# Kernel optimization log

Measured on AMD Instinct MI355X. Metric: run time of the kernel, lower is better.

## Reference

```python
import jax, jax.numpy as jnp
import numpy as np

GRID_LON = 17  # idx = lat*17 + lon in original code


def setup_inputs() -> dict:
    key = jax.random.key(0)
    ks = jax.random.split(key, 16)
    B, S, L = 512, 256, 64
    DIM_RHO, DIM_C, HID = 256, 128, 512
    N_LAT, N_LON = 17, GRID_LON

    rho = jax.random.normal(ks[0], (B, S, DIM_RHO), dtype=jnp.float32)
    c = jax.random.normal(ks[1], (1, DIM_C, N_LAT, N_LON), dtype=jnp.float32)
    w = jax.random.uniform(ks[2], (B, S), dtype=jnp.float32, minval=1e-3, maxval=1.0)
    l = jax.random.uniform(ks[3], (B,), dtype=jnp.float32, minval=0.1, maxval=10.0)
    roads = jax.random.randint(ks[4], (B, L), 0, N_LAT * N_LON)
    lon_idx = jax.random.randint(ks[5], (B, L), 0, N_LON)
    lat_idx = jax.random.randint(ks[6], (B, L), 0, N_LAT)

    sc = lambda fan_in: 1.0 / np.sqrt(fan_in)
    # f2: MLP(128, 256, 128) with selu
    f2_W1 = jax.random.uniform(ks[7], (DIM_C, 256), jnp.float32, -sc(DIM_C), sc(DIM_C))
    f2_b1 = jnp.zeros((256,), jnp.float32)
    f2_W2 = jax.random.uniform(ks[8], (256, DIM_C), jnp.float32, -sc(256), sc(256))
    f2_b2 = jnp.zeros((DIM_C,), jnp.float32)
    # f: MLP2(dim_rho + dim_c, hidden, 1) with selu (use_selu=True)
    fin = DIM_RHO + DIM_C
    f_W1 = jax.random.uniform(ks[9], (fin, HID), jnp.float32, -sc(fin), sc(fin))
    f_b1 = jnp.zeros((HID,), jnp.float32)
    f_W21 = jax.random.uniform(ks[10], (HID, 1), jnp.float32, -sc(HID), sc(HID))
    f_b21 = jnp.zeros((1,), jnp.float32)
    f_W22 = jax.random.uniform(ks[11], (HID, 1), jnp.float32, -sc(HID), sc(HID))
    f_b22 = jnp.zeros((1,), jnp.float32)

    return dict(rho=rho, c=c, w=w, l=l, roads=roads, lon_idx=lon_idx,
                lat_idx=lat_idx, f2_W1=f2_W1, f2_b1=f2_b1, f2_W2=f2_W2,
                f2_b2=f2_b2, f_W1=f_W1, f_b1=f_b1, f_W21=f_W21, f_b21=f_b21,
                f_W22=f_W22, f_b22=f_b22)


def reference(rho, c, w, l, roads, lon_idx, lat_idx,
              f2_W1, f2_b1, f2_W2, f2_b2,
              f_W1, f_b1, f_W21, f_b21, f_W22, f_b22):
    # c: (1, dim_c, n_lat, n_lon) -> (n_lat*n_lon, dim_c)
    c3 = jnp.squeeze(c, 0)                       # (dim_c, n_lat, n_lon)
    c_flat = jnp.transpose(c3, (1, 2, 0)).reshape(-1, c3.shape[0])  # (cells, dim_c)

    # ragged gather-mean, vectorized: (B, L) cell indices -> (B, dim_c)
    idx = lat_idx * GRID_LON + lon_idx           # (B, L)
    c_traj = jnp.mean(c_flat[idx], axis=1)       # (B, dim_c)

    # f2: selu MLP (dropout inactive / eval mode)
    h = jax.nn.selu(c_traj @ f2_W1 + f2_b1)
    c_tr = h @ f2_W2 + f2_b2                     # (B, dim_c)

    # broadcast over seq and concat with rho
    S = rho.shape[1]
    c_exp = jnp.broadcast_to(c_tr[:, None, :], (rho.shape[0], S, c_tr.shape[-1]))
    x = jnp.concatenate([rho, c_exp], axis=2)    # (B, S, dim_rho + dim_c)

    # f (MLP2, selu since use_selu=True)
    h1 = jax.nn.selu(x @ f_W1 + f_b1)            # (B, S, hidden)
    logm = (h1 @ f_W21 + f_b21)[..., 0]          # (B, S)
    logv = (h1 @ f_W22 + f_b22)[..., 0]          # (B, S)

    logw = jnp.log(w)
    logm_agg = jax.nn.logsumexp(logm + logw, axis=1)       # (B,)
    logv_agg = jax.nn.logsumexp(logv + 2.0 * logw, axis=1) # (B,)
    logl = jnp.log(l)
    log_mu = logl - logm_agg
    log_lambda = logl - 3.0 * logm_agg - logv_agg
    return (log_mu, log_lambda)
```

## Files before the change

### kernel.cpp

```cpp
#include <hip/hip_runtime.h>
#include <hip/hip_bf16.h>

typedef short bf16x8 __attribute__((ext_vector_type(8)));
typedef short bf16x4 __attribute__((ext_vector_type(4)));
typedef float f32x4 __attribute__((ext_vector_type(4)));
typedef _Float16 half4 __attribute__((ext_vector_type(4)));

__device__ __forceinline__ short f2bf(float f) {
    union { float f; unsigned u; } v; v.f = f;
    unsigned r = (v.u + 0x7FFFu + ((v.u >> 16) & 1u)) >> 16;
    return (short)r;
}

__device__ __forceinline__ float selu_f(float x) {
    const float scale = 1.0507009873554805f;
    const float sa = 1.0507009873554805f * 1.6732632423543772f;
    return x > 0.f ? scale * x : sa * (__expf(x) - 1.f);
}

__device__ __forceinline__ void gld_lds16(const char* g, char* l) {
    __builtin_amdgcn_global_load_lds(
        (const __attribute__((address_space(1))) unsigned int*)g,
        (__attribute__((address_space(3))) unsigned int*)l, 16, 0, 0);
}

__global__ void __launch_bounds__(512) prep_all_kernel(
    const float* __restrict__ c, const int* __restrict__ lat_idx,
    const int* __restrict__ lon_idx,
    const float* __restrict__ f2W1, const float* __restrict__ f2b1,
    const float* __restrict__ f2W2, const float* __restrict__ f2b2,
    const float* __restrict__ fW1, const float* __restrict__ fb1,
    const float* __restrict__ fW21, const float* __restrict__ fW22,
    short* __restrict__ w1img, _Float16* __restrict__ wvec,
    float* __restrict__ cbias)
{
    const int bid = blockIdx.x;
    const int t = threadIdx.x;

    if (bid < 512) {
        __shared__ int cells[64];
        __shared__ float ctraj[128];
        __shared__ float hbuf[256];
        __shared__ float ctrf[128];
        const int b = bid;

        if (t < 64) cells[t] = lat_idx[b * 64 + t] * 17 + lon_idx[b * 64 + t];
        __syncthreads();

        if (t < 128) {
            float s = 0.f;
            #pragma unroll 8
            for (int j = 0; j < 64; ++j) s += c[t * 289 + cells[j]];
            ctraj[t] = s * (1.f / 64.f);
        }
        __syncthreads();

        if (t < 256) {
            float acc = f2b1[t];
            #pragma unroll 8
            for (int i = 0; i < 128; ++i) acc += ctraj[i] * f2W1[i * 256 + t];
            hbuf[t] = selu_f(acc);
        }
        __syncthreads();

        if (t < 128) {
            float acc = f2b2[t];
            #pragma unroll 8
            for (int i = 0; i < 256; ++i) acc += hbuf[i] * f2W2[i * 128 + t];
            ctrf[t] = acc;
        }
        __syncthreads();

        float acc = fb1[t];
        #pragma unroll 8
        for (int i = 0; i < 128; ++i) acc += ctrf[i] * fW1[(256 + i) * 512 + t];
        cbias[b * 512 + t] = acc;
    } else if (bid < 768) {
        int I = (bid - 512) * 512 + t;
        int e = I & 7;
        int lane = (I >> 3) & 63;
        int cg = (I >> 9) & 31;
        int kc = I >> 14;
        int col = cg * 16 + (lane & 15);
        int k = kc * 32 + ((lane >> 4) << 3) + e;
        w1img[I] = f2bf(fW1[k * 512 + col]);
    } else {
        int I = (bid - 768) * 512 + t;
        int e = I & 3;
        int lane = (I >> 2) & 63;
        int nc = I >> 8;
        int l15 = lane & 15, hi = lane >> 4;
        int n = nc * 16 + hi * 4 + e;
        float v = (l15 == 0) ? fW21[n] : (l15 == 1 ? fW22[n] : 0.f);
        wvec[I] = (_Float16)v;
    }
}

__global__ void __launch_bounds__(1024, 4) fused_gemm_kernel(
    const float* __restrict__ rho, const short* __restrict__ w1img,
    const float* __restrict__ cbias, const _Float16* __restrict__ wvec,
    float* __restrict__ plm, float* __restrict__ plv)
{
    __shared__ __align__(16) char smem[131072];

    const int tid  = threadIdx.x;
    const int lane = tid & 63;
    const int wid  = tid >> 6;
    const int wr   = wid >> 3;
    const int wc2  = wid & 7;
    const int l15  = lane & 15;
    const int hi   = lane >> 4;

    const int b  = blockIdx.x >> 1;
    const int s0 = (blockIdx.x & 1) << 7;

    const int rg_t = tid >> 7;
    const int ln_t = (tid >> 1) & 63;
    const int h_t  = tid & 1;
    const float* prA = rho + (size_t)(b * 256 + s0 + rg_t * 16 + (ln_t & 15)) * 256
                           + ((ln_t >> 4) << 3) + h_t * 4;
    const int awoff = ((rg_t * 64 + ln_t) << 4) + (h_t << 3);

    const char* wsrc = (const char*)w1img;

    f32x4 acc[4][4];
    #pragma unroll
    for (int nf = 0; nf < 4; ++nf)
        #pragma unroll
        for (int sf = 0; sf < 4; ++sf)
            acc[nf][sf] = (f32x4){0.f, 0.f, 0.f, 0.f};

    float4 pf0, pf1;

    {
        const char* bs0 = wsrc + (wid * 2) * 1024 + lane * 16;
        char* bd0 = smem + 24576 + (wid * 2) * 1024;
        gld_lds16(bs0, bd0);
        gld_lds16(bs0 + 1024, bd0 + 1024);
        pf0 = *(const float4*)(prA);
        const char* bs1 = wsrc + 32768 + (wid * 2) * 1024 + lane * 16;
        char* bd1 = smem + 24576 + 32768 + (wid * 2) * 1024;
        gld_lds16(bs1, bd1);
        gld_lds16(bs1 + 1024, bd1 + 1024);
        pf1 = *(const float4*)(prA + 8);
    }

#define CHUNK(I, PFX)                                                          \
    {                                                                          \
        {          \
          bf16x4 hh;                                                           \
          hh[0] = f2bf(PFX.x); hh[1] = f2bf(PFX.y);                            \
          hh[2] = f2bf(PFX.z); hh[3] = f2bf(PFX.w);                            \
          *(bf16x4*)(smem + ((I) % 3) * 8192 + awoff) = hh; }                  \
        if ((I) + 2 <= 7) {    \
            const char* bs = wsrc + ((I) + 2) * 32768 + (wid * 2) * 1024       \
                             + lane * 16;                                      \
            char* bd = smem + 24576 + (((I) + 2) % 3) * 32768                  \
                       + (wid * 2) * 1024;                                     \
            gld_lds16(bs, bd);                                                 \
            gld_lds16(bs + 1024, bd + 1024);                                   \
            PFX = *(const float4*)(prA + ((I) + 2) * 8);                       \
        }                                                                      \
        asm volatile("s_waitcnt lgkmcnt(0)" ::: "memory");                     \
        __builtin_amdgcn_s_barrier();                                          \
        __builtin_amdgcn_sched_barrier(0);                                     \
        {                                                                      \
            bf16x8 aF[4], bF[4];                                               \
            const char* ab = smem + ((I) % 3) * 8192;                          \
            const char* bb = smem + 24576 + ((I) % 3) * 32768;                 \
            _Pragma("unroll")                                                  \
            for (int sf = 0; sf < 4; ++sf)                                     \
                aF[sf] = *(const bf16x8*)(ab + (((wr * 4 + sf) * 64 + lane) << 4)); \
            _Pragma("unroll")                                                  \
            for (int nf = 0; nf < 4; ++nf)                                     \
                bF[nf] = *(const bf16x8*)(bb + (((wc2 * 4 + nf) * 64 + lane) << 4)); \
            _Pragma("unroll")                                                  \
            for (int nf = 0; nf < 4; ++nf)                                     \
                _Pragma("unroll")                                              \
                for (int sf = 0; sf < 4; ++sf)                                 \
                    acc[nf][sf] = __builtin_amdgcn_mfma_f32_16x16x32_bf16(     \
                        bF[nf], aF[sf], acc[nf][sf], 0, 0, 0);                 \
        }                                                                      \
        __builtin_amdgcn_sched_barrier(0);                                     \
        __builtin_amdgcn_s_barrier();                                          \
    }

    CHUNK(0, pf0)
    CHUNK(1, pf1)
    CHUNK(2, pf0)
    CHUNK(3, pf1)
    CHUNK(4, pf0)
    CHUNK(5, pf1)
    CHUNK(6, pf0)
    CHUNK(7, pf1)
#undef CHUNK

    f32x4 rd[4];
    #pragma unroll
    for (int sf = 0; sf < 4; ++sf) rd[sf] = (f32x4){0.f, 0.f, 0.f, 0.f};

    #pragma unroll
    for (int nf = 0; nf < 4; ++nf) {
        f32x4 cbf = *(const f32x4*)(cbias + b * 512 + wc2 * 64 + nf * 16 + hi * 4);
        half4 wv = *(const half4*)(wvec + (size_t)(wc2 * 4 + nf) * 256 + lane * 4);
        #pragma unroll
        for (int sf = 0; sf < 4; ++sf) {
            half4 pa;
            #pragma unroll
            for (int q = 0; q < 4; ++q)
                pa[q] = (_Float16)selu_f(acc[nf][sf][q] + cbf[q]);
            rd[sf] = __builtin_amdgcn_mfma_f32_16x16x16f16(pa, wv, rd[sf], 0, 0, 0);
        }
    }

    float* redM = (float*)(smem + 122880);
    float* redV = (float*)(smem + 126976);
    if (l15 == 0) {
        #pragma unroll
        for (int sf = 0; sf < 4; ++sf)
            *(f32x4*)&redM[wc2 * 128 + wr * 64 + sf * 16 + hi * 4] = rd[sf];
    } else if (l15 == 1) {
        #pragma unroll
        for (int sf = 0; sf < 4; ++sf)
            *(f32x4*)&redV[wc2 * 128 + wr * 64 + sf * 16 + hi * 4] = rd[sf];
    }

    __syncthreads();
    size_t obase = (size_t)b * 256 + s0;
    if (tid < 128) {
        float s = 0.f;
        #pragma unroll
        for (int j = 0; j < 8; ++j) s += redM[j * 128 + tid];
        plm[obase + tid] = s;
    } else if (tid < 256) {
        int rr = tid - 128;
        float s = 0.f;
        #pragma unroll
        for (int j = 0; j < 8; ++j) s += redV[j * 128 + rr];
        plv[obase + rr] = s;
    }
}

__global__ void __launch_bounds__(64) finalize_kernel(
    const float* __restrict__ plm, const float* __restrict__ plv,
    const float* __restrict__ w, const float* __restrict__ l,
    const float* __restrict__ b21p, const float* __restrict__ b22p,
    float* __restrict__ out)
{
    const int b = blockIdx.x;
    const int lane = threadIdx.x;
    const float b21 = b21p[0], b22 = b22p[0];

    float a1[4], a2[4];
    float m1 = -1e30f, m2 = -1e30f;
    #pragma unroll
    for (int i = 0; i < 4; ++i) {
        int s = i * 64 + lane;
        float lw = logf(w[b * 256 + s]);
        a1[i] = plm[b * 256 + s] + b21 + lw;
        a2[i] = plv[b * 256 + s] + b22 + 2.f * lw;
        m1 = fmaxf(m1, a1[i]);
        m2 = fmaxf(m2, a2[i]);
    }
    #pragma unroll
    for (int m = 1; m < 64; m <<= 1) {
        m1 = fmaxf(m1, __shfl_xor(m1, m));
        m2 = fmaxf(m2, __shfl_xor(m2, m));
    }
    float s1 = 0.f, s2 = 0.f;
    #pragma unroll
    for (int i = 0; i < 4; ++i) {
        s1 += expf(a1[i] - m1);
        s2 += expf(a2[i] - m2);
    }
    #pragma unroll
    for (int m = 1; m < 64; m <<= 1) {
        s1 += __shfl_xor(s1, m);
        s2 += __shfl_xor(s2, m);
    }
    if (lane == 0) {
        float lm_agg = m1 + logf(s1);
        float lv_agg = m2 + logf(s2);
        float logl = logf(l[b]);
        out[b]       = logl - lm_agg;
        out[512 + b] = logl - 3.f * lm_agg - lv_agg;
    }
}

extern "C" void kernel_launch(void* const* d_in, const int* in_sizes, int n_in,
                              void* d_out, int out_size, void* d_ws, size_t ws_size,
                              hipStream_t stream) {
    const float* rho     = (const float*)d_in[0];
    const float* c       = (const float*)d_in[1];
    const float* w       = (const float*)d_in[2];
    const float* l       = (const float*)d_in[3];
    const int*   lon_idx = (const int*)d_in[5];
    const int*   lat_idx = (const int*)d_in[6];
    const float* f2W1    = (const float*)d_in[7];
    const float* f2b1    = (const float*)d_in[8];
    const float* f2W2    = (const float*)d_in[9];
    const float* f2b2    = (const float*)d_in[10];
    const float* fW1     = (const float*)d_in[11];
    const float* fb1     = (const float*)d_in[12];
    const float* fW21    = (const float*)d_in[13];
    const float* fb21    = (const float*)d_in[14];
    const float* fW22    = (const float*)d_in[15];
    const float* fb22    = (const float*)d_in[16];
    float* out = (float*)d_out;

    char* ws = (char*)d_ws;
    float*     cbias = (float*)(ws);
    short*     w1img = (short*)(ws + 1048576);
    float*     plm   = (float*)(ws + 1310720);
    float*     plv   = (float*)(ws + 1835008);
    _Float16*  wvec  = (_Float16*)(ws + 2359296);

    prep_all_kernel<<<784, 512, 0, stream>>>(c, lat_idx, lon_idx,
                                             f2W1, f2b1, f2W2, f2b2,
                                             fW1, fb1, fW21, fW22,
                                             w1img, wvec, cbias);
    fused_gemm_kernel<<<1024, 1024, 0, stream>>>(rho, w1img, cbias, wvec,
                                                 plm, plv);
    finalize_kernel<<<512, 64, 0, stream>>>(plm, plv, w, l, fb21, fb22, out);
}
```

Baseline: 99.94 us.

## Split hidden dimension across blocks with smaller double-buffered tiles

```diff
diff --git a/kernel.cpp b/kernel.cpp
--- a/kernel.cpp
+++ b/kernel.cpp
@@ -2,7 +2,6 @@
 #include <hip/hip_bf16.h>
 
 typedef short bf16x8 __attribute__((ext_vector_type(8)));
-typedef short bf16x4 __attribute__((ext_vector_type(4)));
 typedef float f32x4 __attribute__((ext_vector_type(4)));
 typedef _Float16 half4 __attribute__((ext_vector_type(4)));
 
@@ -96,32 +95,32 @@
     }
 }
 
-__global__ void __launch_bounds__(1024, 4) fused_gemm_kernel(
+__global__ void __launch_bounds__(512, 4) fused_gemm_kernel(
     const float* __restrict__ rho, const short* __restrict__ w1img,
     const float* __restrict__ cbias, const _Float16* __restrict__ wvec,
-    float* __restrict__ plm, float* __restrict__ plv)
+    float* __restrict__ plmP, float* __restrict__ plvP)
 {
-    __shared__ __align__(16) char smem[131072];
+    __shared__ __align__(16) char smem[53248];
 
     const int tid  = threadIdx.x;
     const int lane = tid & 63;
     const int wid  = tid >> 6;
-    const int wr   = wid >> 3;
-    const int wc2  = wid & 7;
+    const int wr   = wid >> 2;
+    const int wc   = wid & 3;
     const int l15  = lane & 15;
     const int hi   = lane >> 4;
 
-    const int b  = blockIdx.x >> 1;
-    const int s0 = (blockIdx.x & 1) << 7;
-
-    const int rg_t = tid >> 7;
-    const int ln_t = (tid >> 1) & 63;
-    const int h_t  = tid & 1;
-    const float* prA = rho + (size_t)(b * 256 + s0 + rg_t * 16 + (ln_t & 15)) * 256
-                           + ((ln_t >> 4) << 3) + h_t * 4;
-    const int awoff = ((rg_t * 64 + ln_t) << 4) + (h_t << 3);
-
-    const char* wsrc = (const char*)w1img;
+    const int b  = blockIdx.x >> 2;
+    const int s0 = ((blockIdx.x >> 1) & 1) << 7;
+    const int nh = blockIdx.x & 1;
+
+    const float* prA = rho + (size_t)(b * 256 + s0 + (tid >> 6) * 16 + (tid & 15)) * 256
+                           + (((tid & 63) >> 4) << 3);
+    char* aw = smem + tid * 16;
+
+    const char* wsrc = (const char*)w1img
+                     + ((size_t)(nh * 16 + wid * 2) * 64 + lane) * 16;
+    char* bw = smem + 16384 + (wid * 2) * 1024;
 
     f32x4 acc[4][4];
     #pragma unroll
@@ -130,69 +129,63 @@
         for (int sf = 0; sf < 4; ++sf)
             acc[nf][sf] = (f32x4){0.f, 0.f, 0.f, 0.f};
 
-    float4 pf0, pf1;
-
-    {
-        const char* bs0 = wsrc + (wid * 2) * 1024 + lane * 16;
-        char* bd0 = smem + 24576 + (wid * 2) * 1024;
-        gld_lds16(bs0, bd0);
-        gld_lds16(bs0 + 1024, bd0 + 1024);
-        pf0 = *(const float4*)(prA);
-        const char* bs1 = wsrc + 32768 + (wid * 2) * 1024 + lane * 16;
-        char* bd1 = smem + 24576 + 32768 + (wid * 2) * 1024;
-        gld_lds16(bs1, bd1);
-        gld_lds16(bs1 + 1024, bd1 + 1024);
-        pf1 = *(const float4*)(prA + 8);
-    }
-
-#define CHUNK(I, PFX)                                                          \
+    float4 e0, e1, o0, o1;
+
+    e0 = *(const float4*)(prA);
+    e1 = *(const float4*)(prA + 4);
+    gld_lds16(wsrc, smem + 16384 + (wid * 2) * 1024);
+    gld_lds16(wsrc + 1024, smem + 16384 + (wid * 2) * 1024 + 1024);
+
+#define CHUNK(I, C0, C1, N0, N1, LAST)                                         \
     {                                                                          \
-        {          \
-          bf16x4 hh;                                                           \
-          hh[0] = f2bf(PFX.x); hh[1] = f2bf(PFX.y);                            \
-          hh[2] = f2bf(PFX.z); hh[3] = f2bf(PFX.w);                            \
-          *(bf16x4*)(smem + ((I) % 3) * 8192 + awoff) = hh; }                  \
-        if ((I) + 2 <= 7) {    \
-            const char* bs = wsrc + ((I) + 2) * 32768 + (wid * 2) * 1024       \
-                             + lane * 16;                                      \
-            char* bd = smem + 24576 + (((I) + 2) % 3) * 32768                  \
-                       + (wid * 2) * 1024;                                     \
-            gld_lds16(bs, bd);                                                 \
-            gld_lds16(bs + 1024, bd + 1024);                                   \
-            PFX = *(const float4*)(prA + ((I) + 2) * 8);                       \
+        bf16x8 hh;                                                             \
+        hh[0]=f2bf(C0.x); hh[1]=f2bf(C0.y); hh[2]=f2bf(C0.z); hh[3]=f2bf(C0.w);\
+        hh[4]=f2bf(C1.x); hh[5]=f2bf(C1.y); hh[6]=f2bf(C1.z); hh[7]=f2bf(C1.w);\
+        *(bf16x8*)(aw + ((I)&1) * 8192) = hh;                                  \
+        if (!(LAST)) {                                                         \
+            N0 = *(const float4*)(prA + ((I)+1) * 32);                         \
+            N1 = *(const float4*)(prA + ((I)+1) * 32 + 4);                     \
+            gld_lds16(wsrc + ((I)+1) * 32768,                                  \
+                      bw + (((I)+1)&1) * 16384);                               \
+            gld_lds16(wsrc + ((I)+1) * 32768 + 1024,                           \
+                      bw + (((I)+1)&1) * 16384 + 1024);                        \
         }                                                                      \
         asm volatile("s_waitcnt lgkmcnt(0)" ::: "memory");                     \
+        if (LAST) asm volatile("s_waitcnt vmcnt(0)" ::: "memory");             \
+        else      asm volatile("s_waitcnt vmcnt(4)" ::: "memory");             \
         __builtin_amdgcn_s_barrier();                                          \
         __builtin_amdgcn_sched_barrier(0);                                     \
         {                                                                      \
             bf16x8 aF[4], bF[4];                                               \
-            const char* ab = smem + ((I) % 3) * 8192;                          \
-            const char* bb = smem + 24576 + ((I) % 3) * 32768;                 \
+            const char* ab = smem + ((I)&1) * 8192;                            \
+            const char* bb = smem + 16384 + ((I)&1) * 16384;                   \
             _Pragma("unroll")                                                  \
             for (int sf = 0; sf < 4; ++sf)                                     \
-                aF[sf] = *(const bf16x8*)(ab + (((wr * 4 + sf) * 64 + lane) << 4)); \
+                aF[sf] = *(const bf16x8*)(ab + (((wr*4+sf)*64 + lane) << 4));  \
             _Pragma("unroll")                                                  \
             for (int nf = 0; nf < 4; ++nf)                                     \
-                bF[nf] = *(const bf16x8*)(bb + (((wc2 * 4 + nf) * 64 + lane) << 4)); \
+                bF[nf] = *(const bf16x8*)(bb + (((wc*4+nf)*64 + lane) << 4));  \
+            __builtin_amdgcn_s_setprio(1);                                     \
             _Pragma("unroll")                                                  \
             for (int nf = 0; nf < 4; ++nf)                                     \
                 _Pragma("unroll")                                              \
                 for (int sf = 0; sf < 4; ++sf)                                 \
                     acc[nf][sf] = __builtin_amdgcn_mfma_f32_16x16x32_bf16(     \
                         bF[nf], aF[sf], acc[nf][sf], 0, 0, 0);                 \
+            __builtin_amdgcn_s_setprio(0);                                     \
         }                                                                      \
         __builtin_amdgcn_sched_barrier(0);                                     \
         __builtin_amdgcn_s_barrier();                                          \
     }
 
-    CHUNK(0, pf0)
-    CHUNK(1, pf1)
-    CHUNK(2, pf0)
-    CHUNK(3, pf1)
-    CHUNK(4, pf0)
-    CHUNK(5, pf1)
-    CHUNK(6, pf0)
-    CHUNK(7, pf1)
+    CHUNK(0, e0, e1, o0, o1, false)
+    CHUNK(1, o0, o1, e0, e1, false)
+    CHUNK(2, e0, e1, o0, o1, false)
+    CHUNK(3, o0, o1, e0, e1, false)
+    CHUNK(4, e0, e1, o0, o1, false)
+    CHUNK(5, o0, o1, e0, e1, false)
+    CHUNK(6, e0, e1, o0, o1, false)
+    CHUNK(7, o0, o1, e0, e1, true)
 #undef CHUNK
 
     f32x4 rd[4];
@@ -201,8 +194,9 @@
 
     #pragma unroll
     for (int nf = 0; nf < 4; ++nf) {
-        f32x4 cbf = *(const f32x4*)(cbias + b * 512 + wc2 * 64 + nf * 16 + hi * 4);
-        half4 wv = *(const half4*)(wvec + (size_t)(wc2 * 4 + nf) * 256 + lane * 4);
+        int nc = nh * 16 + wc * 4 + nf;
+        f32x4 cbf = *(const f32x4*)(cbias + b * 512 + nc * 16 + hi * 4);
+        half4 wv = *(const half4*)(wvec + (size_t)nc * 256 + lane * 4);
         #pragma unroll
         for (int sf = 0; sf < 4; ++sf) {
             half4 pa;
@@ -213,36 +207,30 @@
         }
     }
 
-    float* redM = (float*)(smem + 122880);
-    float* redV = (float*)(smem + 126976);
+    float* redM = (float*)(smem + 49152);
+    float* redV = (float*)(smem + 51200);
     if (l15 == 0) {
         #pragma unroll
         for (int sf = 0; sf < 4; ++sf)
-            *(f32x4*)&redM[wc2 * 128 + wr * 64 + sf * 16 + hi * 4] = rd[sf];
+            *(f32x4*)&redM[wc * 128 + wr * 64 + sf * 16 + hi * 4] = rd[sf];
     } else if (l15 == 1) {
         #pragma unroll
         for (int sf = 0; sf < 4; ++sf)
-            *(f32x4*)&redV[wc2 * 128 + wr * 64 + sf * 16 + hi * 4] = rd[sf];
+            *(f32x4*)&redV[wc * 128 + wr * 64 + sf * 16 + hi * 4] = rd[sf];
     }
 
     __syncthreads();
-    size_t obase = (size_t)b * 256 + s0;
+    size_t obase = (size_t)nh * 131072 + (size_t)b * 256 + s0;
     if (tid < 128) {
-        float s = 0.f;
-        #pragma unroll
-        for (int j = 0; j < 8; ++j) s += redM[j * 128 + tid];
-        plm[obase + tid] = s;
+        plmP[obase + tid] = redM[tid] + redM[128 + tid] + redM[256 + tid] + redM[384 + tid];
     } else if (tid < 256) {
         int rr = tid - 128;
-        float s = 0.f;
-        #pragma unroll
-        for (int j = 0; j < 8; ++j) s += redV[j * 128 + rr];
-        plv[obase + rr] = s;
+        plvP[obase + rr] = redV[rr] + redV[128 + rr] + redV[256 + rr] + redV[384 + rr];
     }
 }
 
 __global__ void __launch_bounds__(64) finalize_kernel(
-    const float* __restrict__ plm, const float* __restrict__ plv,
+    const float* __restrict__ plmP, const float* __restrict__ plvP,
     const float* __restrict__ w, const float* __restrict__ l,
     const float* __restrict__ b21p, const float* __restrict__ b22p,
     float* __restrict__ out)
@@ -256,9 +244,10 @@
     #pragma unroll
     for (int i = 0; i < 4; ++i) {
         int s = i * 64 + lane;
-        float lw = logf(w[b * 256 + s]);
-        a1[i] = plm[b * 256 + s] + b21 + lw;
-        a2[i] = plv[b * 256 + s] + b22 + 2.f * lw;
+        int idx = b * 256 + s;
+        float lw = logf(w[idx]);
+        a1[i] = plmP[idx] + plmP[131072 + idx] + b21 + lw;
+        a2[i] = plvP[idx] + plvP[131072 + idx] + b22 + 2.f * lw;
         m1 = fmaxf(m1, a1[i]);
         m2 = fmaxf(m2, a2[i]);
     }
@@ -311,15 +300,15 @@
     char* ws = (char*)d_ws;
     float*     cbias = (float*)(ws);
     short*     w1img = (short*)(ws + 1048576);
-    float*     plm   = (float*)(ws + 1310720);
-    float*     plv   = (float*)(ws + 1835008);
-    _Float16*  wvec  = (_Float16*)(ws + 2359296);
+    float*     plmP  = (float*)(ws + 1310720);
+    float*     plvP  = (float*)(ws + 2359296);
+    _Float16*  wvec  = (_Float16*)(ws + 3407872);
 
     prep_all_kernel<<<784, 512, 0, stream>>>(c, lat_idx, lon_idx,
                                              f2W1, f2b1, f2W2, f2b2,
                                              fW1, fb1, fW21, fW22,
                                              w1img, wvec, cbias);
-    fused_gemm_kernel<<<1024, 1024, 0, stream>>>(rho, w1img, cbias, wvec,
-                                                 plm, plv);
-    finalize_kernel<<<512, 64, 0, stream>>>(plm, plv, w, l, fb21, fb22, out);
-}
+    fused_gemm_kernel<<<2048, 512, 0, stream>>>(rho, w1img, cbias, wvec,
+                                                plmP, plvP);
+    finalize_kernel<<<512, 64, 0, stream>>>(plmP, plvP, w, l, fb21, fb22, out);
+}
```

Result: no change. 101.0 us (+1.0%).
